# Kernel optimization log

Hardware: AMD Instinct MI355X
Metric: run time of the kernel (lower is better)

The kernel has to match this reference:

```python
import jax, jax.numpy as jnp
import numpy as np

B, T, S, H, M, V, L = 16, 128, 256, 512, 512, 32000, 2


def setup_inputs() -> dict:
    key = jax.random.key(0)
    ks = jax.random.split(key, 16)
    s = 0.05
    embed = jax.random.normal(ks[3], (V, H), jnp.float32) * 0.02
    embed = embed.at[0].set(0.0)  # padding_idx=0 row is zero in nn.Embedding
    return {
        'tgt': jax.random.randint(ks[0], (B, T), 0, V),
        'hidden': jax.random.normal(ks[1], (L, B, M), jnp.float32) * 0.1,
        'enc_outs': jax.random.normal(ks[2], (B, S, M), jnp.float32) * 0.1,
        'embed': embed,
        'W_ih0': jax.random.normal(ks[4], (3 * M, H), jnp.float32) * s,
        'W_hh0': jax.random.normal(ks[5], (3 * M, M), jnp.float32) * s,
        'b_ih0': jax.random.normal(ks[6], (3 * M,), jnp.float32) * s,
        'b_hh0': jax.random.normal(ks[7], (3 * M,), jnp.float32) * s,
        'W_ih1': jax.random.normal(ks[8], (3 * M, M), jnp.float32) * s,
        'W_hh1': jax.random.normal(ks[9], (3 * M, M), jnp.float32) * s,
        'b_ih1': jax.random.normal(ks[10], (3 * M,), jnp.float32) * s,
        'b_hh1': jax.random.normal(ks[11], (3 * M,), jnp.float32) * s,
        'W_out': jax.random.normal(ks[12], (V, M), jnp.float32) * s,
        'b_out': jax.random.normal(ks[13], (V,), jnp.float32) * s,
    }


def _gru_layer(x, h0, W_ih, W_hh, b_ih, b_hh):
    """PyTorch-convention GRU layer. x: [B,T,in], h0: [B,M] -> (ys [B,T,M], hT [B,M])."""
    # precompute input-side gates for all timesteps: [B,T,3M]
    xg = jnp.einsum('bti,gi->btg', x, W_ih) + b_ih

    def step(h, xg_t):
        gh = h @ W_hh.T + b_hh
        i_r, i_z, i_n = jnp.split(xg_t, 3, axis=-1)
        h_r, h_z, h_n = jnp.split(gh, 3, axis=-1)
        r = jax.nn.sigmoid(i_r + h_r)
        z = jax.nn.sigmoid(i_z + h_z)
        n = jnp.tanh(i_n + r * h_n)
        h_new = (1.0 - z) * n + z * h
        return h_new, h_new

    hT, ys = jax.lax.scan(step, h0, jnp.swapaxes(xg, 0, 1))  # scan over time
    return jnp.swapaxes(ys, 0, 1), hT


def reference(tgt, hidden, enc_outs, embed, W_ih0, W_hh0, b_ih0, b_hh0,
              W_ih1, W_hh1, b_ih1, b_hh1, W_out, b_out):
    x = embed[tgt]  # [B,T,H]
    out0, h0f = _gru_layer(x, hidden[0], W_ih0, W_hh0, b_ih0, b_hh0)
    outputs, h1f = _gru_layer(out0, hidden[1], W_ih1, W_hh1, b_ih1, b_hh1)  # [B,T,M]
    hn = jnp.stack([h0f, h1f])  # [L,B,M]
    cn = jnp.zeros_like(hn)
    # dot-product attention, batched over all timesteps (fuses the per-ts Python loop)
    scores = jnp.einsum('btm,bsm->bts', outputs, enc_outs)
    weights = jax.nn.softmax(scores, axis=-1)
    contexts = jnp.einsum('bts,bsm->btm', weights, enc_outs)
    attn_outs = outputs + contexts
    logits = jnp.einsum('btm,vm->btv', attn_outs, W_out) + b_out  # dropout p=0 -> identity
    return logits, (hn, cn)
```

## Files before the change

### kernel.cpp

```cpp
#include <hip/hip_runtime.h>
#include <hip/hip_bf16.h>
#include <math.h>

#define B_ 16
#define T_ 128
#define S_ 256
#define H_ 512
#define M_ 512
#define V_ 32000
#define SENT 0x7FC0DEADu

typedef __attribute__((ext_vector_type(8))) short short8v;
typedef __attribute__((ext_vector_type(4))) float float4v;

__global__ __launch_bounds__(512) void k_fill(unsigned int* __restrict__ p, int n)
{
  const int i = blockIdx.x * 512 + threadIdx.x;
  if (i < n) p[i] = SENT;
}

__global__ __launch_bounds__(256) void k_xg_bf16(const int* __restrict__ tgt,
    const float* __restrict__ embed, const float* __restrict__ Bm,
    const float* __restrict__ bias, float* __restrict__ C)
{
  __shared__ unsigned short As[128 * 40];
  __shared__ unsigned short Bs[128 * 40];
  const int tid = threadIdx.x;
  const int nbase = blockIdx.x * 128;
  const int mbase = blockIdx.y * 128;
  const int wv = tid >> 6;
  const int l  = tid & 63;
  const int wr = wv >> 1, wc = wv & 1;
  const int r = l & 15, q = l >> 4;

  const int row0 = tid >> 2, row1 = (tid + 256) >> 2;
  const int v0 = tgt[mbase + row0];
  const int v1 = tgt[mbase + row1];

  float4v acc[4][4];
#pragma unroll
  for (int mi = 0; mi < 4; ++mi)
#pragma unroll
    for (int ni = 0; ni < 4; ++ni)
      acc[mi][ni] = (float4v){0.f, 0.f, 0.f, 0.f};

  for (int k0 = 0; k0 < 512; k0 += 32) {
    __syncthreads();
#pragma unroll
    for (int h = 0; h < 2; ++h) {
      const int c = tid + h * 256;
      const int row = h ? row1 : row0;
      const int av  = h ? v1 : v0;
      const int cb = c & 3;
      const float* Ag = embed + (size_t)av * 512 + k0 + cb * 8;
      float4 f0 = *(const float4*)(Ag);
      float4 f1 = *(const float4*)(Ag + 4);
      union { short8v v; __hip_bfloat162 h2[4]; } pa;
      pa.h2[0] = __float22bfloat162_rn({f0.x, f0.y});
      pa.h2[1] = __float22bfloat162_rn({f0.z, f0.w});
      pa.h2[2] = __float22bfloat162_rn({f1.x, f1.y});
      pa.h2[3] = __float22bfloat162_rn({f1.z, f1.w});
      *(short8v*)&As[row * 40 + cb * 8] = pa.v;
      const float* Bg = Bm + (size_t)(nbase + row) * 512 + k0 + cb * 8;
      float4 g0 = *(const float4*)(Bg);
      float4 g1 = *(const float4*)(Bg + 4);
      union { short8v v; __hip_bfloat162 h2[4]; } pb;
      pb.h2[0] = __float22bfloat162_rn({g0.x, g0.y});
      pb.h2[1] = __float22bfloat162_rn({g0.z, g0.w});
      pb.h2[2] = __float22bfloat162_rn({g1.x, g1.y});
      pb.h2[3] = __float22bfloat162_rn({g1.z, g1.w});
      *(short8v*)&Bs[row * 40 + cb * 8] = pb.v;
    }
    __syncthreads();

    short8v af[4], bf[4];
#pragma unroll
    for (int mi = 0; mi < 4; ++mi)
      af[mi] = *(short8v*)&As[(wr * 64 + mi * 16 + r) * 40 + q * 8];
#pragma unroll
    for (int ni = 0; ni < 4; ++ni)
      bf[ni] = *(short8v*)&Bs[(wc * 64 + ni * 16 + r) * 40 + q * 8];
#pragma unroll
    for (int mi = 0; mi < 4; ++mi)
#pragma unroll
      for (int ni = 0; ni < 4; ++ni)
        acc[mi][ni] = __builtin_amdgcn_mfma_f32_16x16x32_bf16(af[mi], bf[ni], acc[mi][ni], 0, 0, 0);
  }

  const int mg = mbase + wr * 64;
  const int ng = nbase + wc * 64;
#pragma unroll
  for (int ni = 0; ni < 4; ++ni) {
    const int col = ng + ni * 16 + r;
    const float bj = bias[col];
#pragma unroll
    for (int mi = 0; mi < 4; ++mi) {
      const int rowb = mg + mi * 16 + q * 4;
      float4v v = acc[mi][ni];
      C[(size_t)(rowb + 0) * 1536 + col] = v[0] + bj;
      C[(size_t)(rowb + 1) * 1536 + col] = v[1] + bj;
      C[(size_t)(rowb + 2) * 1536 + col] = v[2] + bj;
      C[(size_t)(rowb + 3) * 1536 + col] = v[3] + bj;
    }
  }
}

struct F4x8 { float4 a, b, c, d, e, f, g, h; };
__device__ inline F4x8 bulk8_ld(const float* rowbase, int sc)
{
  F4x8 r;
  const float* p = rowbase + sc * 4;
  asm volatile(
    "global_load_dwordx4 %0, %[p], off sc0 sc1\n\t"
    "global_load_dwordx4 %1, %[p], off offset:256 sc0 sc1\n\t"
    "global_load_dwordx4 %2, %[p], off offset:512 sc0 sc1\n\t"
    "global_load_dwordx4 %3, %[p], off offset:768 sc0 sc1\n\t"
    "global_load_dwordx4 %4, %[p], off offset:1024 sc0 sc1\n\t"
    "global_load_dwordx4 %5, %[p], off offset:1280 sc0 sc1\n\t"
    "global_load_dwordx4 %6, %[p], off offset:1536 sc0 sc1\n\t"
    "global_load_dwordx4 %7, %[p], off offset:1792 sc0 sc1\n\t"
    "s_waitcnt vmcnt(0)"
    : "=&v"(r.a), "=&v"(r.b), "=&v"(r.c), "=&v"(r.d),
      "=&v"(r.e), "=&v"(r.f), "=&v"(r.g), "=&v"(r.h)
    : [p]"v"(p)
    : "memory");
  return r;
}

__device__ inline void bulk16_ld(const float* r0base, const float* r1base, int sc,
                                 F4x8& x, F4x8& y)
{
  const float* p0 = r0base + sc * 4;
  const float* p1 = r1base + sc * 4;
  asm volatile(
    "global_load_dwordx4 %0, %[p0], off sc0 sc1\n\t"
    "global_load_dwordx4 %1, %[p0], off offset:256 sc0 sc1\n\t"
    "global_load_dwordx4 %2, %[p0], off offset:512 sc0 sc1\n\t"
    "global_load_dwordx4 %3, %[p0], off offset:768 sc0 sc1\n\t"
    "global_load_dwordx4 %4, %[p0], off offset:1024 sc0 sc1\n\t"
    "global_load_dwordx4 %5, %[p0], off offset:1280 sc0 sc1\n\t"
    "global_load_dwordx4 %6, %[p0], off offset:1536 sc0 sc1\n\t"
    "global_load_dwordx4 %7, %[p0], off offset:1792 sc0 sc1\n\t"
    "global_load_dwordx4 %8, %[p1], off sc0 sc1\n\t"
    "global_load_dwordx4 %9, %[p1], off offset:256 sc0 sc1\n\t"
    "global_load_dwordx4 %10, %[p1], off offset:512 sc0 sc1\n\t"
    "global_load_dwordx4 %11, %[p1], off offset:768 sc0 sc1\n\t"
    "global_load_dwordx4 %12, %[p1], off offset:1024 sc0 sc1\n\t"
    "global_load_dwordx4 %13, %[p1], off offset:1280 sc0 sc1\n\t"
    "global_load_dwordx4 %14, %[p1], off offset:1536 sc0 sc1\n\t"
    "global_load_dwordx4 %15, %[p1], off offset:1792 sc0 sc1\n\t"
    "s_waitcnt vmcnt(0)"
    : "=&v"(x.a), "=&v"(x.b), "=&v"(x.c), "=&v"(x.d),
      "=&v"(x.e), "=&v"(x.f), "=&v"(x.g), "=&v"(x.h),
      "=&v"(y.a), "=&v"(y.b), "=&v"(y.c), "=&v"(y.d),
      "=&v"(y.e), "=&v"(y.f), "=&v"(y.g), "=&v"(y.h)
    : [p0]"v"(p0), [p1]"v"(p1)
    : "memory");
}

__device__ inline bool anysent(const F4x8& r)
{
  auto c1 = [](float4 v) {
    return (__float_as_uint(v.x) == SENT) | (__float_as_uint(v.y) == SENT) |
           (__float_as_uint(v.z) == SENT) | (__float_as_uint(v.w) == SENT);
  };
  return c1(r.a) | c1(r.b) | c1(r.c) | c1(r.d) |
         c1(r.e) | c1(r.f) | c1(r.g) | c1(r.h);
}

__device__ inline void f4x8_store(const F4x8& r, int sc, float* dstrow)
{
  *(float4*)&dstrow[(0*16 + sc) * 4] = r.a;
  *(float4*)&dstrow[(1*16 + sc) * 4] = r.b;
  *(float4*)&dstrow[(2*16 + sc) * 4] = r.c;
  *(float4*)&dstrow[(3*16 + sc) * 4] = r.d;
  *(float4*)&dstrow[(4*16 + sc) * 4] = r.e;
  *(float4*)&dstrow[(5*16 + sc) * 4] = r.f;
  *(float4*)&dstrow[(6*16 + sc) * 4] = r.g;
  *(float4*)&dstrow[(7*16 + sc) * 4] = r.h;
}

__device__ inline void stage_sent(const float* rowbase, int sc, float* dstrow)
{
  F4x8 r = bulk8_ld(rowbase, sc);
  while (anysent(r)) {
    __builtin_amdgcn_s_sleep(1);
    r = bulk8_ld(rowbase, sc);
  }
  f4x8_store(r, sc, dstrow);
}

__device__ inline void stage2_sent(const float* r0base, const float* r1base,
                                   int sc, float* d0, float* d1)
{
  F4x8 x, y;
  bulk16_ld(r0base, r1base, sc, x, y);
  while (anysent(x)) {
    __builtin_amdgcn_s_sleep(1);
    x = bulk8_ld(r0base, sc);
  }
  f4x8_store(x, sc, d0);
  while (anysent(y)) {
    __builtin_amdgcn_s_sleep(1);
    y = bulk8_ld(r1base, sc);
  }
  f4x8_store(y, sc, d1);
}

__global__ __launch_bounds__(256) void k_gru2(
    const float* __restrict__ xg0,
    const float* __restrict__ Whh0, const float* __restrict__ bhh0,
    const float* __restrict__ Wih1, const float* __restrict__ bih1,
    const float* __restrict__ Whh1, const float* __restrict__ bhh1,
    const float* __restrict__ hidden,
    float* __restrict__ out0, float* __restrict__ y1, float* __restrict__ hn)
{
  __shared__ float Wl[24][520];
  __shared__ float hx[2][16 * 520];
  __shared__ float ps[24][16][17];
  const int bid = blockIdx.x;
  const int lt = threadIdx.x;

  if (bid >= 192) {
    __shared__ int done;
    if (lt == 0) done = 0;
    __syncthreads();
    const float* flag = y1 + (size_t)(15 * T_ + 127) * 512 + 511;
    float a0 = 1.0f + lt, a1 = 2.0f + lt, a2 = 3.0f, a3 = 4.0f;
    const float mb = 1.0001f, cb = 0.9999f;
    for (;;) {
#pragma unroll 16
      for (int i = 0; i < 512; ++i) {
        a0 = __builtin_fmaf(a0, mb, cb); a1 = __builtin_fmaf(a1, mb, cb);
        a2 = __builtin_fmaf(a2, mb, cb); a3 = __builtin_fmaf(a3, mb, cb);
      }
      if (lt == 0 &&
          __float_as_uint(__hip_atomic_load(flag, __ATOMIC_RELAXED,
                                            __HIP_MEMORY_SCOPE_AGENT)) != SENT)
        done = 1;
      __syncthreads();
      if (done) break;
    }
    asm volatile("" :: "v"(a0), "v"(a1), "v"(a2), "v"(a3));
    return;
  }

  const bool isB = bid >= 64;
  const int wg = isB ? bid - 64 : bid;
  const int dbase = isB ? wg * 4 : wg * 8;

  for (int r = 0; r < 24; ++r) {
    const float* src;
    if (!isB) src = Whh0 + (size_t)((r >> 3) * 512 + dbase + (r & 7)) * 512;
    else if (r < 12) src = Whh1 + (size_t)((r >> 2) * 512 + dbase + (r & 3)) * 512;
    else { int rr = r - 12; src = Wih1 + (size_t)((rr >> 2) * 512 + dbase + (rr & 3)) * 512; }
    Wl[r][lt] = src[lt];
    Wl[r][lt + 256] = src[lt + 256];
  }

  const int kq = lt & 15;
  const int bq = (lt >> 4) & 3;
  const int rgrp = lt >> 6;
  const int sb = lt >> 4;
  const int sc = lt & 15;
  float* ybuf = isB ? y1 : out0;
  const float* h0g = hidden + (isB ? 8192 : 0);

  const int rb = isB ? (lt >> 2) : (lt >> 3);
  const int rdl = isB ? (lt & 3) : (lt & 7);
  const int rdg = dbase + rdl;
  const int nred = isB ? 64 : 128;
  float bhr = 0.f, bhz = 0.f, bhn = 0.f, bir = 0.f, biz = 0.f, bin_ = 0.f;
  if (lt < nred) {
    const float* bhh = isB ? bhh1 : bhh0;
    bhr = bhh[rdg]; bhz = bhh[512 + rdg]; bhn = bhh[1024 + rdg];
    if (isB) { bir = bih1[rdg]; biz = bih1[512 + rdg]; bin_ = bih1[1024 + rdg]; }
  }
  __syncthreads();

  for (int t = 0; t < T_; ++t) {
    float pxr = 0.f, pxz = 0.f, pxn = 0.f;
    if (!isB && lt < 128) {
      const float* xrow = xg0 + (size_t)(rb * T_ + t) * 1536;
      pxr = xrow[rdg]; pxz = xrow[512 + rdg]; pxn = xrow[1024 + rdg];
    }

    if (t == 0) {
#pragma unroll
      for (int j = 0; j < 8; ++j)
        *(float4*)&hx[0][sb * 520 + (j * 16 + sc) * 4] =
            *(const float4*)(h0g + sb * 512 + (j * 16 + sc) * 4);
      if (isB)
        stage_sent(out0 + (size_t)(sb * T_) * 512, sc, &hx[1][sb * 520]);
    } else if (!isB) {
      stage_sent(ybuf + (size_t)(sb * T_ + t - 1) * 512, sc, &hx[0][sb * 520]);
    } else {
      stage2_sent(ybuf + (size_t)(sb * T_ + t - 1) * 512,
                  out0 + (size_t)(sb * T_ + t) * 512,
                  sc, &hx[0][sb * 520], &hx[1][sb * 520]);
    }
    __syncthreads();

    const float* inb = (isB && rgrp >= 2) ? &hx[1][0] : &hx[0][0];
    float acc[6][4];
#pragma unroll
    for (int jr = 0; jr < 6; ++jr)
#pragma unroll
      for (int jb = 0; jb < 4; ++jb) acc[jr][jb] = 0.f;
#pragma unroll
    for (int i = 0; i < 8; ++i) {
      const int kb = kq * 4 + i * 64;
      float4 hv0 = *(const float4*)(inb + (bq * 4 + 0) * 520 + kb);
      float4 hv1 = *(const float4*)(inb + (bq * 4 + 1) * 520 + kb);
      float4 hv2 = *(const float4*)(inb + (bq * 4 + 2) * 520 + kb);
      float4 hv3 = *(const float4*)(inb + (bq * 4 + 3) * 520 + kb);
#pragma unroll
      for (int jr = 0; jr < 6; ++jr) {
        float4 wv = *(const float4*)(&Wl[rgrp * 6 + jr][kb]);
        acc[jr][0] += wv.x*hv0.x + wv.y*hv0.y + wv.z*hv0.z + wv.w*hv0.w;
        acc[jr][1] += wv.x*hv1.x + wv.y*hv1.y + wv.z*hv1.z + wv.w*hv1.w;
        acc[jr][2] += wv.x*hv2.x + wv.y*hv2.y + wv.z*hv2.z + wv.w*hv2.w;
        acc[jr][3] += wv.x*hv3.x + wv.y*hv3.y + wv.z*hv3.z + wv.w*hv3.w;
      }
    }
#pragma unroll
    for (int jr = 0; jr < 6; ++jr)
#pragma unroll
      for (int jb = 0; jb < 4; ++jb)
        ps[rgrp * 6 + jr][bq * 4 + jb][kq] = acc[jr][jb];
    __syncthreads();

    if (lt < nred) {
      float ghr, ghz, ghn, ixr, ixz, ixn;
      if (!isB) {
        float s0 = 0.f, s1 = 0.f, s2 = 0.f;
#pragma unroll
        for (int q = 0; q < 16; ++q) {
          s0 += ps[rdl][rb][q];
          s1 += ps[8 + rdl][rb][q];
          s2 += ps[16 + rdl][rb][q];
        }
        ghr = s0 + bhr; ghz = s1 + bhz; ghn = s2 + bhn;
        ixr = pxr; ixz = pxz; ixn = pxn;
      } else {
        float s0=0.f,s1=0.f,s2=0.f,s3=0.f,s4=0.f,s5=0.f;
#pragma unroll
        for (int q = 0; q < 16; ++q) {
          s0 += ps[rdl][rb][q];       s1 += ps[4 + rdl][rb][q];  s2 += ps[8 + rdl][rb][q];
          s3 += ps[12 + rdl][rb][q];  s4 += ps[16 + rdl][rb][q]; s5 += ps[20 + rdl][rb][q];
        }
        ghr = s0 + bhr; ghz = s1 + bhz; ghn = s2 + bhn;
        ixr = s3 + bir; ixz = s4 + biz; ixn = s5 + bin_;
      }
      float rr = 1.f / (1.f + expf(-(ixr + ghr)));
      float zz = 1.f / (1.f + expf(-(ixz + ghz)));
      float nn = tanhf(ixn + rr * ghn);
      float hp = hx[0][rb * 520 + rdg];
      float hnew = (1.f - zz) * nn + zz * hp;
      __hip_atomic_store(&ybuf[(size_t)(rb * T_ + t) * 512 + rdg], hnew,
                         __ATOMIC_RELAXED, __HIP_MEMORY_SCOPE_AGENT);
      if (t == T_ - 1) hn[(isB ? 8192 : 0) + rb * 512 + rdg] = hnew;
    }
    __syncthreads();
  }
}

__global__ __launch_bounds__(256) void k_attn(const float* __restrict__ y,
    const float* __restrict__ enc, float* __restrict__ aout)
{
  __shared__ float orow[512];
  __shared__ float wbuf[256];
  __shared__ float red[8];
  const int row = blockIdx.x;
  const int b = row >> 7;
  const int lt = threadIdx.x;
  orow[lt]       = y[(size_t)row*512 + lt];
  orow[lt + 256] = y[(size_t)row*512 + lt + 256];
  __syncthreads();
  const float* er = enc + (size_t)(b*S_ + lt) * 512;
  float acc = 0.f;
  for (int k = 0; k < 512; k += 4) {
    float4 e = *(const float4*)(er + k);
    acc += orow[k]*e.x + orow[k+1]*e.y + orow[k+2]*e.z + orow[k+3]*e.w;
  }
  float m = acc;
#pragma unroll
  for (int off = 32; off > 0; off >>= 1) m = fmaxf(m, __shfl_down(m, off));
  if ((lt & 63) == 0) red[lt >> 6] = m;
  __syncthreads();
  float mx = fmaxf(fmaxf(red[0], red[1]), fmaxf(red[2], red[3]));
  float e = expf(acc - mx);
  wbuf[lt] = e;
  float s = e;
#pragma unroll
  for (int off = 32; off > 0; off >>= 1) s += __shfl_down(s, off);
  if ((lt & 63) == 0) red[4 + (lt >> 6)] = s;
  __syncthreads();
  const float inv = 1.f / (red[4] + red[5] + red[6] + red[7]);
  const int kk = lt * 2;
  float c0 = 0.f, c1 = 0.f;
  for (int s2 = 0; s2 < S_; ++s2) {
    float ws = wbuf[s2];
    float2 ev = *(const float2*)(enc + (size_t)(b*S_ + s2)*512 + kk);
    c0 += ws * ev.x; c1 += ws * ev.y;
  }
  aout[(size_t)row*512 + kk]     = orow[kk]     + c0 * inv;
  aout[(size_t)row*512 + kk + 1] = orow[kk + 1] + c1 * inv;
}

__global__ __launch_bounds__(256) void k_logits(const float* __restrict__ A,
    const float* __restrict__ Bm, const float* __restrict__ bias,
    float* __restrict__ C)
{
  __shared__ unsigned short Bs[128 * 512];
  __shared__ unsigned short As[128 * 64];
  const int tid = threadIdx.x;
  const int nbase = blockIdx.x * 128;
  const int wv = tid >> 6;
  const int l  = tid & 63;
  const int wr = wv >> 1, wc = wv & 1;
  const int r = l & 15, q = l >> 4;

  for (int i = 0; i < 32; ++i) {
    const int gid = tid + i * 256;
    const int row = gid >> 6, cg = gid & 63;
    const float* Bg = Bm + (size_t)(nbase + row) * 512 + cg * 8;
    float4 g0 = *(const float4*)(Bg);
    float4 g1 = *(const float4*)(Bg + 4);
    union { short8v v; __hip_bfloat162 h2[4]; } pb;
    pb.h2[0] = __float22bfloat162_rn({g0.x, g0.y});
    pb.h2[1] = __float22bfloat162_rn({g0.z, g0.w});
    pb.h2[2] = __float22bfloat162_rn({g1.x, g1.y});
    pb.h2[3] = __float22bfloat162_rn({g1.z, g1.w});
    const int byte = (row * 1024 + cg * 16) ^ ((row & 7) << 4);
    *(short8v*)&Bs[byte >> 1] = pb.v;
  }
  __syncthreads();

  for (int m = 0; m < 16; ++m) {
    const int mbase = m * 128;
    float4v acc[4][4];
#pragma unroll
    for (int mi = 0; mi < 4; ++mi)
#pragma unroll
      for (int ni = 0; ni < 4; ++ni)
        acc[mi][ni] = (float4v){0.f, 0.f, 0.f, 0.f};

    for (int kc = 0; kc < 8; ++kc) {
#pragma unroll
      for (int i = 0; i < 4; ++i) {
        const int gid = tid + i * 256;
        const int row = gid >> 3, cg = gid & 7;
        const float* Ag = A + (size_t)(mbase + row) * 512 + kc * 64 + cg * 8;
        float4 f0 = *(const float4*)(Ag);
        float4 f1 = *(const float4*)(Ag + 4);
        union { short8v v; __hip_bfloat162 h2[4]; } pa;
        pa.h2[0] = __float22bfloat162_rn({f0.x, f0.y});
        pa.h2[1] = __float22bfloat162_rn({f0.z, f0.w});
        pa.h2[2] = __float22bfloat162_rn({f1.x, f1.y});
        pa.h2[3] = __float22bfloat162_rn({f1.z, f1.w});
        const int byte = (row * 128 + cg * 16) ^ ((row & 7) << 4);
        *(short8v*)&As[byte >> 1] = pa.v;
      }
      __syncthreads();

#pragma unroll
      for (int k0s = 0; k0s < 2; ++k0s) {
        short8v af[4], bf[4];
#pragma unroll
        for (int mi = 0; mi < 4; ++mi) {
          const int row = wr * 64 + mi * 16 + r;
          const int byte = (row * 128 + k0s * 64 + q * 16) ^ ((row & 7) << 4);
          af[mi] = *(short8v*)&As[byte >> 1];
        }
#pragma unroll
        for (int ni = 0; ni < 4; ++ni) {
          const int row = wc * 64 + ni * 16 + r;
          const int byte = (row * 1024 + kc * 128 + k0s * 64 + q * 16) ^ ((row & 7) << 4);
          bf[ni] = *(short8v*)&Bs[byte >> 1];
        }
#pragma unroll
        for (int mi = 0; mi < 4; ++mi)
#pragma unroll
          for (int ni = 0; ni < 4; ++ni)
            acc[mi][ni] = __builtin_amdgcn_mfma_f32_16x16x32_bf16(af[mi], bf[ni], acc[mi][ni], 0, 0, 0);
      }
      __syncthreads();
    }

    const int mg = mbase + wr * 64;
    const int ng = nbase + wc * 64;
#pragma unroll
    for (int ni = 0; ni < 4; ++ni) {
      const int col = ng + ni * 16 + r;
      const float bj = bias[col];
#pragma unroll
      for (int mi = 0; mi < 4; ++mi) {
        const int rowb = mg + mi * 16 + q * 4;
        float4v v = acc[mi][ni];
        C[(size_t)(rowb + 0) * V_ + col] = v[0] + bj;
        C[(size_t)(rowb + 1) * V_ + col] = v[1] + bj;
        C[(size_t)(rowb + 2) * V_ + col] = v[2] + bj;
        C[(size_t)(rowb + 3) * V_ + col] = v[3] + bj;
      }
    }
  }
}

extern "C" void kernel_launch(void* const* d_in, const int* in_sizes, int n_in,
                              void* d_out, int out_size, void* d_ws, size_t ws_size,
                              hipStream_t stream)
{
  const int*   tgt    = (const int*)  d_in[0];
  const float* hidden = (const float*)d_in[1];
  const float* enc    = (const float*)d_in[2];
  const float* embed  = (const float*)d_in[3];
  const float* W_ih0  = (const float*)d_in[4];
  const float* W_hh0  = (const float*)d_in[5];
  const float* b_ih0  = (const float*)d_in[6];
  const float* b_hh0  = (const float*)d_in[7];
  const float* W_ih1  = (const float*)d_in[8];
  const float* W_hh1  = (const float*)d_in[9];
  const float* b_ih1  = (const float*)d_in[10];
  const float* b_hh1  = (const float*)d_in[11];
  const float* W_out  = (const float*)d_in[12];
  const float* b_out  = (const float*)d_in[13];
  float* out = (float*)d_out;

  float* ws   = (float*)d_ws;
  float* xbuf = ws;
  float* xg   = ws + 1048576;
  float* out0 = xg + 3145728;
  float* y1   = out0 + 1048576;

  const size_t logitsN = (size_t)(B_*T_) * V_;
  float* hn = out + logitsN;
  float* cn = hn + 16384;

  hipMemsetAsync(cn, 0, (size_t)16384 * sizeof(float), stream);

  k_fill<<<dim3(4096), dim3(512), 0, stream>>>((unsigned int*)out0, 2097152);
  k_xg_bf16<<<dim3(1536/128, 2048/128), dim3(256), 0, stream>>>(tgt, embed, W_ih0, b_ih0, xg);
  k_gru2<<<dim3(256), dim3(256), 0, stream>>>(xg, W_hh0, b_hh0, W_ih1, b_ih1,
                                              W_hh1, b_hh1, hidden, out0, y1, hn);
  k_attn<<<dim3(B_*T_), dim3(256), 0, stream>>>(y1, enc, xbuf);
  k_logits<<<dim3(V_/128), dim3(256), 0, stream>>>(xbuf, W_out, b_out, out);
}
```

Measured before the change: 1.305 ms.

## Emit bf16 attention output and load A fragments directly from global in logits GEMM

The attention kernel now converts its output to bf16 when it writes it, instead of storing fp32. The logits GEMM then reads A fragments straight from global/L2 into registers, dropping the per-k-chunk LDS staging, the fp32-to-bf16 conversion and the two barriers per chunk. This removes redundant conversion work repeated across all 250 column blocks and halves the bytes read for A. The cost is uncoalesced, per-lane 16-byte global loads whose latency is no longer hidden by shared-memory staging.

Result: no change. 1.301 ms, median of 2 (-0.3%).

```diff
diff --git a/kernel.cpp b/kernel.cpp
--- a/kernel.cpp
+++ b/kernel.cpp
@@ -366,7 +366,7 @@
 }
 
 __global__ __launch_bounds__(256) void k_attn(const float* __restrict__ y,
-    const float* __restrict__ enc, float* __restrict__ aout)
+    const float* __restrict__ enc, __hip_bfloat162* __restrict__ abf)
 {
   __shared__ float orow[512];
   __shared__ float wbuf[256];
@@ -404,16 +404,15 @@
     float2 ev = *(const float2*)(enc + (size_t)(b*S_ + s2)*512 + kk);
     c0 += ws * ev.x; c1 += ws * ev.y;
   }
-  aout[(size_t)row*512 + kk]     = orow[kk]     + c0 * inv;
-  aout[(size_t)row*512 + kk + 1] = orow[kk + 1] + c1 * inv;
-}
-
-__global__ __launch_bounds__(256) void k_logits(const float* __restrict__ A,
+  abf[(size_t)row * 256 + lt] =
+      __float22bfloat162_rn({orow[kk] + c0 * inv, orow[kk + 1] + c1 * inv});
+}
+
+__global__ __launch_bounds__(256) void k_logits(const unsigned short* __restrict__ Abf,
     const float* __restrict__ Bm, const float* __restrict__ bias,
     float* __restrict__ C)
 {
   __shared__ unsigned short Bs[128 * 512];
-  __shared__ unsigned short As[128 * 64];
   const int tid = threadIdx.x;
   const int nbase = blockIdx.x * 128;
   const int wv = tid >> 6;
@@ -437,8 +436,13 @@
   }
   __syncthreads();
 
+  const unsigned short* arow[4];
+#pragma unroll
+  for (int mi = 0; mi < 4; ++mi)
+    arow[mi] = Abf + (size_t)(wr * 64 + mi * 16 + r) * 512 + q * 8;
+
   for (int m = 0; m < 16; ++m) {
-    const int mbase = m * 128;
+    const size_t moff = (size_t)m * 128 * 512;
     float4v acc[4][4];
 #pragma unroll
     for (int mi = 0; mi < 4; ++mi)
@@ -446,33 +450,17 @@
       for (int ni = 0; ni < 4; ++ni)
         acc[mi][ni] = (float4v){0.f, 0.f, 0.f, 0.f};
 
+#pragma unroll 2
     for (int kc = 0; kc < 8; ++kc) {
-#pragma unroll
-      for (int i = 0; i < 4; ++i) {
-        const int gid = tid + i * 256;
-        const int row = gid >> 3, cg = gid & 7;
-        const float* Ag = A + (size_t)(mbase + row) * 512 + kc * 64 + cg * 8;
-        float4 f0 = *(const float4*)(Ag);
-        float4 f1 = *(const float4*)(Ag + 4);
-        union { short8v v; __hip_bfloat162 h2[4]; } pa;
-        pa.h2[0] = __float22bfloat162_rn({f0.x, f0.y});
-        pa.h2[1] = __float22bfloat162_rn({f0.z, f0.w});
-        pa.h2[2] = __float22bfloat162_rn({f1.x, f1.y});
-        pa.h2[3] = __float22bfloat162_rn({f1.z, f1.w});
-        const int byte = (row * 128 + cg * 16) ^ ((row & 7) << 4);
-        *(short8v*)&As[byte >> 1] = pa.v;
-      }
-      __syncthreads();
-
+      short8v af[2][4];
+#pragma unroll
+      for (int k0s = 0; k0s < 2; ++k0s)
+#pragma unroll
+        for (int mi = 0; mi < 4; ++mi)
+          af[k0s][mi] = *(const short8v*)(arow[mi] + moff + kc * 64 + k0s * 32);
 #pragma unroll
       for (int k0s = 0; k0s < 2; ++k0s) {
-        short8v af[4], bf[4];
-#pragma unroll
-        for (int mi = 0; mi < 4; ++mi) {
-          const int row = wr * 64 + mi * 16 + r;
-          const int byte = (row * 128 + k0s * 64 + q * 16) ^ ((row & 7) << 4);
-          af[mi] = *(short8v*)&As[byte >> 1];
-        }
+        short8v bf[4];
 #pragma unroll
         for (int ni = 0; ni < 4; ++ni) {
           const int row = wc * 64 + ni * 16 + r;
@@ -483,12 +471,11 @@
         for (int mi = 0; mi < 4; ++mi)
 #pragma unroll
           for (int ni = 0; ni < 4; ++ni)
-            acc[mi][ni] = __builtin_amdgcn_mfma_f32_16x16x32_bf16(af[mi], bf[ni], acc[mi][ni], 0, 0, 0);
+            acc[mi][ni] = __builtin_amdgcn_mfma_f32_16x16x32_bf16(af[k0s][mi], bf[ni], acc[mi][ni], 0, 0, 0);
       }
-      __syncthreads();
-    }
-
-    const int mg = mbase + wr * 64;
+    }
+
+    const int mg = m * 128 + wr * 64;
     const int ng = nbase + wc * 64;
 #pragma unroll
     for (int ni = 0; ni < 4; ++ni) {
@@ -528,7 +515,7 @@
   float* out = (float*)d_out;
 
   float* ws   = (float*)d_ws;
-  float* xbuf = ws;
+  __hip_bfloat162* abf = (__hip_bfloat162*)ws;
   float* xg   = ws + 1048576;
   float* out0 = xg + 3145728;
   float* y1   = out0 + 1048576;
@@ -543,6 +530,7 @@
   k_xg_bf16<<<dim3(1536/128, 2048/128), dim3(256), 0, stream>>>(tgt, embed, W_ih0, b_ih0, xg);
   k_gru2<<<dim3(256), dim3(256), 0, stream>>>(xg, W_hh0, b_hh0, W_ih1, b_ih1,
                                               W_hh1, b_hh1, hidden, out0, y1, hn);
-  k_attn<<<dim3(B_*T_), dim3(256), 0, stream>>>(y1, enc, xbuf);
-  k_logits<<<dim3(V_/128), dim3(256), 0, stream>>>(xbuf, W_out, b_out, out);
-}
+  k_attn<<<dim3(B_*T_), dim3(256), 0, stream>>>(y1, enc, abf);
+  k_logits<<<dim3(V_/128), dim3(256), 0, stream>>>((const unsigned short*)abf,
+                                                   W_out, b_out, out);
+}
```
